# Optimization experiments

Measured on AMD Instinct MI355X. Metric: run time of the kernel, lower is better.

The kernel has to match this reference:

```python
import jax, jax.numpy as jnp
import numpy as np

D_IN = 512
N_EXPERTS = 32
HID = 16
BATCH = 262144


def setup_inputs() -> dict:
    key = jax.random.key(0)
    kx, kg, k1, kb1, k2, kb2 = jax.random.split(key, 6)
    x = jax.random.normal(kx, (BATCH, D_IN), dtype=jnp.float32)
    # gating: n_experts independent Linear(d_in, 1, bias=False) -> [E, d_in]
    Wg = jax.random.normal(kg, (N_EXPERTS, D_IN), dtype=jnp.float32) * 0.02
    # experts: Linear(d_in,16) -> GELU -> Linear(16,1)
    W1 = jax.random.normal(k1, (N_EXPERTS, D_IN, HID), dtype=jnp.float32) * 0.02
    b1 = jax.random.normal(kb1, (N_EXPERTS, HID), dtype=jnp.float32) * 0.02
    W2 = jax.random.normal(k2, (N_EXPERTS, HID), dtype=jnp.float32) * 0.02
    b2 = jax.random.normal(kb2, (N_EXPERTS,), dtype=jnp.float32) * 0.02
    return {"x": x, "Wg": Wg, "W1": W1, "b1": b1, "W2": W2, "b2": b2}


def reference(x, Wg, W1, b1, W2, b2):
    # gating scores for all experts at once: [B, E]
    gating = jnp.einsum("bd,ed->be", x, Wg)
    gate = jax.nn.softmax(gating, axis=1)  # softmax over experts (torch dim=1)
    # all experts' first layer in one batched GEMM: [B, E, HID]
    h = jax.nn.gelu(jnp.einsum("bd,edh->beh", x, W1) + b1, approximate=False)
    # second layer collapses HID -> scalar per expert: [B, E]
    out = jnp.einsum("beh,eh->be", h, W2) + b2
    # bmm([B,1,E],[B,E,1]) == weighted sum over experts -> [B, 1]
    xi = jnp.sum(out * gate, axis=1, keepdims=True)
    return xi
```

## Files before the change

kernel.cpp:

```cpp
#include <hip/hip_runtime.h>
#include <hip/hip_bf16.h>

#define D_IN 512
#define NEXP 32
#define HID 16
#define NT 34
#define KSTEPS 16
#define BM 128
#define BATCH 262144
#define LDGX 129
#define SPW 5

typedef __attribute__((ext_vector_type(8))) short bfrag;
typedef __attribute__((ext_vector_type(4))) float f32x4;

__device__ inline ushort f2bf(float f) {
  uint32_t u = __float_as_uint(f);
  u += 0x7fffu + ((u >> 16) & 1u);
  return (ushort)(u >> 16);
}

__device__ inline bfrag cvt8(const float4 a, const float4 b) {
  union { bfrag v; uint u[4]; } r;
  asm("v_cvt_pk_bf16_f32 %0, %1, %2" : "=v"(r.u[0]) : "v"(a.x), "v"(a.y));
  asm("v_cvt_pk_bf16_f32 %0, %1, %2" : "=v"(r.u[1]) : "v"(a.z), "v"(a.w));
  asm("v_cvt_pk_bf16_f32 %0, %1, %2" : "=v"(r.u[2]) : "v"(b.x), "v"(b.y));
  asm("v_cvt_pk_bf16_f32 %0, %1, %2" : "=v"(r.u[3]) : "v"(b.z), "v"(b.w));
  return r.v;
}

__device__ inline float gelu_t(float v) {
  float t = 0.7978845608028654f * fmaf(0.044715f * v * v, v, v);
  t = fminf(fmaxf(t, -9.f), 9.f);
  float e = __expf(-2.f * t);
  float th = (1.f - e) * __builtin_amdgcn_rcpf(1.f + e);
  return 0.5f * v * (1.f + th);
}

__device__ inline void gload_lds16(const ushort* g, ushort* l) {
  __builtin_amdgcn_global_load_lds(
      (const __attribute__((address_space(1))) void*)g,
      (__attribute__((address_space(3))) void*)l, 16, 0, 0);
}

__global__ void prepack_kernel(const float* __restrict__ Wg,
                               const float* __restrict__ W1,
                               ushort* __restrict__ P) {
  int tid = blockIdx.x * 256 + threadIdx.x;
  const int total = KSTEPS * NT * 64;
  if (tid >= total) return;
  int l  = tid & 63;
  int t  = (tid >> 6) % NT;
  int ks = tid / (NT * 64);
  int n  = t * 16 + (l & 15);
  int kb = ks * 32 + (l >> 4) * 8;
  __align__(16) ushort v[8];
#pragma unroll
  for (int j = 0; j < 8; ++j) {
    int k = kb + j;
    float w;
    if (n < NEXP) {
      w = Wg[n * D_IN + k];
    } else {
      int e = (n - 32) >> 4, h = (n - 32) & 15;
      w = W1[(e * D_IN + k) * HID + h];
    }
    v[j] = f2bf(w);
  }
  *reinterpret_cast<int4*>(P + (size_t)tid * 8) = *reinterpret_cast<const int4*>(v);
}

__global__ __launch_bounds__(512, 2)
void moe_kernel(const float* __restrict__ x, const ushort* __restrict__ P,
                const float* __restrict__ b1, const float* __restrict__ W2,
                const float* __restrict__ b2, float* __restrict__ out) {
  __shared__ __align__(16) ushort Blds[3][NT * 512];
  __shared__ float gxl[17 * LDGX];
  __shared__ float p0l[BM];
  __shared__ float sl[BM];

  const int tid = threadIdx.x;
  const int l = tid & 63;
  const int wid = tid >> 6;
  const int wm = wid >> 1, wn = wid & 1;
  const int lane16 = l & 15, lg = l >> 4;
  const size_t rowBase = (size_t)blockIdx.x * BM;

  int stg[SPW];
#pragma unroll
  for (int i = 0; i < SPW; ++i) {
    int t = wid * SPW + i;
    stg[i] = (t >= NT) ? (t - NT) : t;
  }

  f32x4 acc[2][17];
#pragma unroll
  for (int f = 0; f < 2; ++f)
#pragma unroll
    for (int t = 0; t < 17; ++t) acc[f][t] = (f32x4){0.f, 0.f, 0.f, 0.f};

  const float* xp0 = x + (rowBase + wm * 32 + lane16) * D_IN + lg * 8;
  const float* xp1 = xp0 + 16 * D_IN;

  float4 abuf[2][4];

  abuf[0][0] = *reinterpret_cast<const float4*>(xp0);
  abuf[0][1] = *reinterpret_cast<const float4*>(xp0 + 4);
  abuf[0][2] = *reinterpret_cast<const float4*>(xp1);
  abuf[0][3] = *reinterpret_cast<const float4*>(xp1 + 4);
#pragma unroll
  for (int g = 0; g < 2; ++g)
#pragma unroll
    for (int i = 0; i < SPW; ++i)
      gload_lds16(P + ((size_t)(g * NT + stg[i]) * 64 + l) * 8,
                  &Blds[g][stg[i] * 512]);
  asm volatile("s_waitcnt vmcnt(5)" ::: "memory");
  __builtin_amdgcn_s_barrier();

#pragma unroll
  for (int ks = 0; ks < KSTEPS; ++ks) {
    const int cur = ks & 1, nxt = cur ^ 1;
    const int rb = ks % 3;
    const bfrag a0 = cvt8(abuf[cur][0], abuf[cur][1]);
    const bfrag a1 = cvt8(abuf[cur][2], abuf[cur][3]);
    if (ks < KSTEPS - 1) {
      abuf[nxt][0] = *reinterpret_cast<const float4*>(xp0 + (ks + 1) * 32);
      abuf[nxt][1] = *reinterpret_cast<const float4*>(xp0 + (ks + 1) * 32 + 4);
      abuf[nxt][2] = *reinterpret_cast<const float4*>(xp1 + (ks + 1) * 32);
      abuf[nxt][3] = *reinterpret_cast<const float4*>(xp1 + (ks + 1) * 32 + 4);
    }
    if (ks < KSTEPS - 2) {
      const int wb = (ks + 2) % 3;
#pragma unroll
      for (int i = 0; i < SPW; ++i)
        gload_lds16(P + ((size_t)((ks + 2) * NT + stg[i]) * 64 + l) * 8,
                    &Blds[wb][stg[i] * 512]);
    }
#pragma unroll
    for (int t = 0; t < 17; ++t) {
      const bfrag b = *reinterpret_cast<const bfrag*>(
          &Blds[rb][(wn * 17 + t) * 512 + l * 8]);
      acc[0][t] = __builtin_amdgcn_mfma_f32_16x16x32_bf16(b, a0, acc[0][t], 0, 0, 0);
      acc[1][t] = __builtin_amdgcn_mfma_f32_16x16x32_bf16(b, a1, acc[1][t], 0, 0, 0);
    }
    if (ks < KSTEPS - 1) {
      if (ks < KSTEPS - 2)
        asm volatile("s_waitcnt vmcnt(9)" ::: "memory");
      else
        asm volatile("s_waitcnt vmcnt(4)" ::: "memory");
      __builtin_amdgcn_s_barrier();
    }
  }

  const int row0 = wm * 32 + lane16;
  float oreg[17][2];

  if (wn == 0) {
    float gh[2][8];
    float pac[2] = {0.f, 0.f};
#pragma unroll
    for (int f = 0; f < 2; ++f) {
      const int row = row0 + f * 16;
      float mx = fmaxf(fmaxf(fmaxf(acc[f][0][0], acc[f][0][1]), fmaxf(acc[f][0][2], acc[f][0][3])),
                       fmaxf(fmaxf(acc[f][1][0], acc[f][1][1]), fmaxf(acc[f][1][2], acc[f][1][3])));
      mx = fmaxf(mx, __shfl_xor(mx, 16));
      mx = fmaxf(mx, __shfl_xor(mx, 32));
      float sum = 0.f;
#pragma unroll
      for (int t = 0; t < 2; ++t)
#pragma unroll
        for (int r = 0; r < 4; ++r) {
          float g = __expf(acc[f][t][r] - mx);
          gh[f][t * 4 + r] = g;
          sum += g;
        }
      sum += __shfl_xor(sum, 16);
      sum += __shfl_xor(sum, 32);
      if (lg == 0) sl[row] = sum;
      if (lg == 3) gxl[row] = gh[f][3];
#pragma unroll
      for (int r = 0; r < 4; ++r)
        gxl[(1 + lg * 4 + r) * LDGX + row] = gh[f][4 + r];
    }
#pragma unroll
    for (int t = 2; t < 17; ++t) {
      const int e = t - 2;
      const float4 b1v = *reinterpret_cast<const float4*>(b1 + e * HID + lg * 4);
      const float4 w2v = *reinterpret_cast<const float4*>(W2 + e * HID + lg * 4);
      const float b2v = b2[e];
#pragma unroll
      for (int f = 0; f < 2; ++f) {
        float p = gelu_t(acc[f][t][0] + b1v.x) * w2v.x;
        p = fmaf(gelu_t(acc[f][t][1] + b1v.y), w2v.y, p);
        p = fmaf(gelu_t(acc[f][t][2] + b1v.z), w2v.z, p);
        p = fmaf(gelu_t(acc[f][t][3] + b1v.w), w2v.w, p);
        p += __shfl_xor(p, 16);
        p += __shfl_xor(p, 32);
        if (lg == (e >> 2)) pac[f] = fmaf(p + b2v, gh[f][e & 3], pac[f]);
      }
    }
#pragma unroll
    for (int f = 0; f < 2; ++f) {
      float p0 = pac[f];
      p0 += __shfl_xor(p0, 16);
      p0 += __shfl_xor(p0, 32);
      if (lg == 0) p0l[row0 + f * 16] = p0;
    }
  } else {
#pragma unroll
    for (int t = 0; t < 17; ++t) {
      const int e = t + 15;
      const float4 b1v = *reinterpret_cast<const float4*>(b1 + e * HID + lg * 4);
      const float4 w2v = *reinterpret_cast<const float4*>(W2 + e * HID + lg * 4);
      const float b2v = b2[e];
#pragma unroll
      for (int f = 0; f < 2; ++f) {
        float p = gelu_t(acc[f][t][0] + b1v.x) * w2v.x;
        p = fmaf(gelu_t(acc[f][t][1] + b1v.y), w2v.y, p);
        p = fmaf(gelu_t(acc[f][t][2] + b1v.z), w2v.z, p);
        p = fmaf(gelu_t(acc[f][t][3] + b1v.w), w2v.w, p);
        p += __shfl_xor(p, 16);
        p += __shfl_xor(p, 32);
        oreg[t][f] = p + b2v;
      }
    }
  }

  __syncthreads();
  if (wn == 1) {
#pragma unroll
    for (int f = 0; f < 2; ++f) {
      const int row = row0 + f * 16;
      float a = p0l[row];
#pragma unroll
      for (int t = 0; t < 17; ++t)
        a = fmaf(oreg[t][f], gxl[t * LDGX + row], a);
      if (lg == 0) out[rowBase + row] = a / sl[row];
    }
  }
}

extern "C" void kernel_launch(void* const* d_in, const int* in_sizes, int n_in,
                              void* d_out, int out_size, void* d_ws, size_t ws_size,
                              hipStream_t stream) {
  const float* x  = (const float*)d_in[0];
  const float* Wg = (const float*)d_in[1];
  const float* W1 = (const float*)d_in[2];
  const float* b1 = (const float*)d_in[3];
  const float* W2 = (const float*)d_in[4];
  const float* b2 = (const float*)d_in[5];
  float* out = (float*)d_out;
  ushort* P = (ushort*)d_ws;

  hipLaunchKernelGGL(prepack_kernel, dim3((KSTEPS * NT * 64 + 255) / 256), dim3(256),
                     0, stream, Wg, W1, P);
  hipLaunchKernelGGL(moe_kernel, dim3(BATCH / BM), dim3(512),
                     0, stream, x, P, b1, W2, b2, out);
}
```

Measured before the change: 332.6 us.

## Retile MFMA warps to 2x4 grid with 64 rows and 9 tiles each

The 8 waves were arranged 4 rows by 2 column groups (32 rows x 17 tiles). They are now arranged 2 by 4 (64 rows x 8-9 tiles), so each B fragment read from LDS feeds four MFMAs instead of two. This lowers LDS read traffic per MFMA, at the cost of more global x loads per wave. The epilogue is also restructured: wave column 0 writes all gate probabilities to shared memory, then every wave computes its own experts' GELU and weighted sum, and partial sums are reduced across four slots. This replaces the earlier lopsided two-wave epilogue and adds an extra barrier.

Result: slower. 421.9 us (+26.9%).

```diff
diff --git a/kernel.cpp b/kernel.cpp
--- a/kernel.cpp
+++ b/kernel.cpp
@@ -8,7 +8,7 @@
 #define KSTEPS 16
 #define BM 128
 #define BATCH 262144
-#define LDGX 129
+#define GXLA 129
 #define SPW 5
 
 typedef __attribute__((ext_vector_type(8))) short bfrag;
@@ -75,16 +75,19 @@
                 const float* __restrict__ b1, const float* __restrict__ W2,
                 const float* __restrict__ b2, float* __restrict__ out) {
   __shared__ __align__(16) ushort Blds[3][NT * 512];
-  __shared__ float gxl[17 * LDGX];
-  __shared__ float p0l[BM];
+  __shared__ float gall[NEXP * GXLA];
+  __shared__ float pp[4][BM];
   __shared__ float sl[BM];
 
   const int tid = threadIdx.x;
   const int l = tid & 63;
   const int wid = tid >> 6;
-  const int wm = wid >> 1, wn = wid & 1;
+  const int wm = wid & 1;
+  const int wn = wid >> 1;
   const int lane16 = l & 15, lg = l >> 4;
   const size_t rowBase = (size_t)blockIdx.x * BM;
+  const int tbase = wn * 9 - (wn == 3);
+  const int ntile = (wn < 2) ? 9 : 8;
 
   int stg[SPW];
 #pragma unroll
@@ -93,21 +96,21 @@
     stg[i] = (t >= NT) ? (t - NT) : t;
   }
 
-  f32x4 acc[2][17];
-#pragma unroll
-  for (int f = 0; f < 2; ++f)
-#pragma unroll
-    for (int t = 0; t < 17; ++t) acc[f][t] = (f32x4){0.f, 0.f, 0.f, 0.f};
-
-  const float* xp0 = x + (rowBase + wm * 32 + lane16) * D_IN + lg * 8;
-  const float* xp1 = xp0 + 16 * D_IN;
-
-  float4 abuf[2][4];
-
-  abuf[0][0] = *reinterpret_cast<const float4*>(xp0);
-  abuf[0][1] = *reinterpret_cast<const float4*>(xp0 + 4);
-  abuf[0][2] = *reinterpret_cast<const float4*>(xp1);
-  abuf[0][3] = *reinterpret_cast<const float4*>(xp1 + 4);
+  f32x4 acc[4][9];
+#pragma unroll
+  for (int f = 0; f < 4; ++f)
+#pragma unroll
+    for (int i = 0; i < 9; ++i) acc[f][i] = (f32x4){0.f, 0.f, 0.f, 0.f};
+
+  const float* xr = x + (rowBase + wm * 64 + lane16) * D_IN + lg * 8;
+
+  float4 abuf[8];
+
+#pragma unroll
+  for (int f = 0; f < 4; ++f) {
+    abuf[f * 2]     = *reinterpret_cast<const float4*>(xr + f * 16 * D_IN);
+    abuf[f * 2 + 1] = *reinterpret_cast<const float4*>(xr + f * 16 * D_IN + 4);
+  }
 #pragma unroll
   for (int g = 0; g < 2; ++g)
 #pragma unroll
@@ -119,15 +122,16 @@
 
 #pragma unroll
   for (int ks = 0; ks < KSTEPS; ++ks) {
-    const int cur = ks & 1, nxt = cur ^ 1;
     const int rb = ks % 3;
-    const bfrag a0 = cvt8(abuf[cur][0], abuf[cur][1]);
-    const bfrag a1 = cvt8(abuf[cur][2], abuf[cur][3]);
+    bfrag a[4];
+#pragma unroll
+    for (int f = 0; f < 4; ++f) a[f] = cvt8(abuf[f * 2], abuf[f * 2 + 1]);
     if (ks < KSTEPS - 1) {
-      abuf[nxt][0] = *reinterpret_cast<const float4*>(xp0 + (ks + 1) * 32);
-      abuf[nxt][1] = *reinterpret_cast<const float4*>(xp0 + (ks + 1) * 32 + 4);
-      abuf[nxt][2] = *reinterpret_cast<const float4*>(xp1 + (ks + 1) * 32);
-      abuf[nxt][3] = *reinterpret_cast<const float4*>(xp1 + (ks + 1) * 32 + 4);
+#pragma unroll
+      for (int f = 0; f < 4; ++f) {
+        abuf[f * 2]     = *reinterpret_cast<const float4*>(xr + f * 16 * D_IN + (ks + 1) * 32);
+        abuf[f * 2 + 1] = *reinterpret_cast<const float4*>(xr + f * 16 * D_IN + (ks + 1) * 32 + 4);
+      }
     }
     if (ks < KSTEPS - 2) {
       const int wb = (ks + 2) % 3;
@@ -137,29 +141,29 @@
                     &Blds[wb][stg[i] * 512]);
     }
 #pragma unroll
-    for (int t = 0; t < 17; ++t) {
-      const bfrag b = *reinterpret_cast<const bfrag*>(
-          &Blds[rb][(wn * 17 + t) * 512 + l * 8]);
-      acc[0][t] = __builtin_amdgcn_mfma_f32_16x16x32_bf16(b, a0, acc[0][t], 0, 0, 0);
-      acc[1][t] = __builtin_amdgcn_mfma_f32_16x16x32_bf16(b, a1, acc[1][t], 0, 0, 0);
+    for (int i = 0; i < 9; ++i) {
+      if (i < ntile) {
+        const bfrag b = *reinterpret_cast<const bfrag*>(
+            &Blds[rb][(tbase + i) * 512 + (l << 3)]);
+#pragma unroll
+        for (int f = 0; f < 4; ++f)
+          acc[f][i] = __builtin_amdgcn_mfma_f32_16x16x32_bf16(b, a[f], acc[f][i], 0, 0, 0);
+      }
     }
     if (ks < KSTEPS - 1) {
       if (ks < KSTEPS - 2)
-        asm volatile("s_waitcnt vmcnt(9)" ::: "memory");
+        asm volatile("s_waitcnt vmcnt(13)" ::: "memory");
       else
-        asm volatile("s_waitcnt vmcnt(4)" ::: "memory");
+        asm volatile("s_waitcnt vmcnt(8)" ::: "memory");
       __builtin_amdgcn_s_barrier();
     }
   }
 
-  const int row0 = wm * 32 + lane16;
-  float oreg[17][2];
+  const int row0 = wm * 64 + lane16;
 
   if (wn == 0) {
-    float gh[2][8];
-    float pac[2] = {0.f, 0.f};
-#pragma unroll
-    for (int f = 0; f < 2; ++f) {
+#pragma unroll
+    for (int f = 0; f < 4; ++f) {
       const int row = row0 + f * 16;
       float mx = fmaxf(fmaxf(fmaxf(acc[f][0][0], acc[f][0][1]), fmaxf(acc[f][0][2], acc[f][0][3])),
                        fmaxf(fmaxf(acc[f][1][0], acc[f][1][1]), fmaxf(acc[f][1][2], acc[f][1][3])));
@@ -171,72 +175,45 @@
 #pragma unroll
         for (int r = 0; r < 4; ++r) {
           float g = __expf(acc[f][t][r] - mx);
-          gh[f][t * 4 + r] = g;
           sum += g;
+          gall[(t * 16 + lg * 4 + r) * GXLA + row] = g;
         }
       sum += __shfl_xor(sum, 16);
       sum += __shfl_xor(sum, 32);
       if (lg == 0) sl[row] = sum;
-      if (lg == 3) gxl[row] = gh[f][3];
-#pragma unroll
-      for (int r = 0; r < 4; ++r)
-        gxl[(1 + lg * 4 + r) * LDGX + row] = gh[f][4 + r];
-    }
-#pragma unroll
-    for (int t = 2; t < 17; ++t) {
-      const int e = t - 2;
+    }
+  }
+  __syncthreads();
+
+  float pacc[4] = {0.f, 0.f, 0.f, 0.f};
+#pragma unroll
+  for (int i = 0; i < 9; ++i) {
+    const bool valid = (i < ntile) && ((wn != 0) || (i >= 2));
+    if (valid) {
+      const int e = tbase + i - 2;
       const float4 b1v = *reinterpret_cast<const float4*>(b1 + e * HID + lg * 4);
       const float4 w2v = *reinterpret_cast<const float4*>(W2 + e * HID + lg * 4);
       const float b2v = b2[e];
 #pragma unroll
-      for (int f = 0; f < 2; ++f) {
-        float p = gelu_t(acc[f][t][0] + b1v.x) * w2v.x;
-        p = fmaf(gelu_t(acc[f][t][1] + b1v.y), w2v.y, p);
-        p = fmaf(gelu_t(acc[f][t][2] + b1v.z), w2v.z, p);
-        p = fmaf(gelu_t(acc[f][t][3] + b1v.w), w2v.w, p);
+      for (int f = 0; f < 4; ++f) {
+        float p = gelu_t(acc[f][i][0] + b1v.x) * w2v.x;
+        p = fmaf(gelu_t(acc[f][i][1] + b1v.y), w2v.y, p);
+        p = fmaf(gelu_t(acc[f][i][2] + b1v.z), w2v.z, p);
+        p = fmaf(gelu_t(acc[f][i][3] + b1v.w), w2v.w, p);
         p += __shfl_xor(p, 16);
         p += __shfl_xor(p, 32);
-        if (lg == (e >> 2)) pac[f] = fmaf(p + b2v, gh[f][e & 3], pac[f]);
+        pacc[f] = fmaf(p + b2v, gall[e * GXLA + row0 + f * 16], pacc[f]);
       }
     }
-#pragma unroll
-    for (int f = 0; f < 2; ++f) {
-      float p0 = pac[f];
-      p0 += __shfl_xor(p0, 16);
-      p0 += __shfl_xor(p0, 32);
-      if (lg == 0) p0l[row0 + f * 16] = p0;
-    }
-  } else {
-#pragma unroll
-    for (int t = 0; t < 17; ++t) {
-      const int e = t + 15;
-      const float4 b1v = *reinterpret_cast<const float4*>(b1 + e * HID + lg * 4);
-      const float4 w2v = *reinterpret_cast<const float4*>(W2 + e * HID + lg * 4);
-      const float b2v = b2[e];
-#pragma unroll
-      for (int f = 0; f < 2; ++f) {
-        float p = gelu_t(acc[f][t][0] + b1v.x) * w2v.x;
-        p = fmaf(gelu_t(acc[f][t][1] + b1v.y), w2v.y, p);
-        p = fmaf(gelu_t(acc[f][t][2] + b1v.z), w2v.z, p);
-        p = fmaf(gelu_t(acc[f][t][3] + b1v.w), w2v.w, p);
-        p += __shfl_xor(p, 16);
-        p += __shfl_xor(p, 32);
-        oreg[t][f] = p + b2v;
-      }
-    }
-  }
-
+  }
+  if (lg == 0) {
+#pragma unroll
+    for (int f = 0; f < 4; ++f) pp[wn][row0 + f * 16] = pacc[f];
+  }
   __syncthreads();
-  if (wn == 1) {
-#pragma unroll
-    for (int f = 0; f < 2; ++f) {
-      const int row = row0 + f * 16;
-      float a = p0l[row];
-#pragma unroll
-      for (int t = 0; t < 17; ++t)
-        a = fmaf(oreg[t][f], gxl[t * LDGX + row], a);
-      if (lg == 0) out[rowBase + row] = a / sl[row];
-    }
+  if (tid < BM) {
+    float a = pp[0][tid] + pp[1][tid] + pp[2][tid] + pp[3][tid];
+    out[rowBase + tid] = a / sl[tid];
   }
 }
 
```
